# Kernel tuning notes

Measured on AMD Instinct MI355X. Metric: run time of the kernel, lower is better.

The kernel has to match this reference:

```python
import jax, jax.numpy as jnp
import numpy as np

B, C, H, W = 16, 256, 112, 112
WS, HEADS, HIDDEN = 7, 4, 512  # window_size, num_heads, int(dim*mlp_ratio)
EPS = 1e-5


def _layernorm(x, g, b):
    m = jnp.mean(x, axis=-1, keepdims=True)
    v = jnp.mean(jnp.square(x - m), axis=-1, keepdims=True)
    return (x - m) * jax.lax.rsqrt(v + EPS) * g + b


def setup_inputs() -> dict:
    key = jax.random.key(0)
    ks = jax.random.split(key, 6)
    s = 0.02
    return {
        "x": jax.random.normal(ks[0], (B, C, H, W), jnp.float32),
        "ln1_g": jnp.ones((C,), jnp.float32),
        "ln1_b": jnp.zeros((C,), jnp.float32),
        "qkv_w": jax.random.normal(ks[1], (C, 3 * C), jnp.float32) * s,
        "qkv_b": jnp.zeros((3 * C,), jnp.float32),
        "proj_w": jax.random.normal(ks[2], (C, C), jnp.float32) * s,
        "proj_b": jnp.zeros((C,), jnp.float32),
        "ln2_g": jnp.ones((C,), jnp.float32),
        "ln2_b": jnp.zeros((C,), jnp.float32),
        "mlp_w1": jax.random.normal(ks[3], (C, HIDDEN), jnp.float32) * s,
        "mlp_b1": jnp.zeros((HIDDEN,), jnp.float32),
        "mlp_w2": jax.random.normal(ks[4], (HIDDEN, C), jnp.float32) * s,
        "mlp_b2": jnp.zeros((C,), jnp.float32),
    }


def reference(x, ln1_g, ln1_b, qkv_w, qkv_b, proj_w, proj_b,
              ln2_g, ln2_b, mlp_w1, mlp_b1, mlp_w2, mlp_b2):
    nh, nw = H // WS, W // WS  # H,W divisible by WS -> no padding branch
    T = WS * WS               # 49 tokens per window
    d = C // HEADS
    # window partition: (B,C,H,W) -> (B*nh*nw, T, C)
    win = x.reshape(B, C, nh, WS, nw, WS).transpose(0, 2, 4, 3, 5, 1)
    win = win.reshape(B * nh * nw, T, C)
    # LN1 + MHA (pytorch nn.MultiheadAttention semantics)
    n1 = _layernorm(win, ln1_g, ln1_b)
    qkv = n1 @ qkv_w + qkv_b
    q, k, v = jnp.split(qkv, 3, axis=-1)
    N = win.shape[0]
    q = q.reshape(N, T, HEADS, d)
    k = k.reshape(N, T, HEADS, d)
    v = v.reshape(N, T, HEADS, d)
    scores = jnp.einsum('nthd,nshd->nhts', q, k) / jnp.sqrt(jnp.float32(d))
    attn = jax.nn.softmax(scores, axis=-1)
    o = jnp.einsum('nhts,nshd->nthd', attn, v).reshape(N, T, C)
    o = o @ proj_w + proj_b
    win = win + o
    # LN2 + MLP (exact erf GELU, matching nn.GELU default)
    n2 = _layernorm(win, ln2_g, ln2_b)
    hmid = jax.nn.gelu(n2 @ mlp_w1 + mlp_b1, approximate=False)
    win = win + (hmid @ mlp_w2 + mlp_b2)
    # window reverse: (B*nh*nw, T, C) -> (B,C,H,W)
    y = win.reshape(B, nh, nw, WS, WS, C).transpose(0, 5, 1, 3, 2, 4)
    return y.reshape(B, C, H, W)
```

## Files before the change

kernel.cpp:

```cpp
#include <hip/hip_runtime.h>
#include <hip/hip_bf16.h>

typedef __bf16 bf16x8 __attribute__((ext_vector_type(8)));
typedef float  f32x4  __attribute__((ext_vector_type(4)));
typedef unsigned short u16x8 __attribute__((ext_vector_type(8)));

#define CH    256
#define IMG   112
#define WSZ   7
#define TOK   49
#define NWIN  4096
#define HID   512
#define NTHR  512

#define SX_ST 260

#define OFF_AF   51200
#define OFF_V    51200
#define OFF_Q    83968
#define OFF_P    83968
#define PSZ      7168
#define OFF_HM   83968
#define OFF_K    116736
#define OFF_OF   116736
#define OFF_MR   149504
#define OFF_PRM  150016
#define OFF_PART 154112
#define SMEM_SZ  157248

#define WS_PROJ_BLK 384
#define WS_W1_BLK   512
#define WS_W2_BLK   768

__device__ __forceinline__ unsigned short f2bf(float f) {
    __bf16 h = (__bf16)f;
    return __builtin_bit_cast(unsigned short, h);
}

__device__ __forceinline__ f32x4 mfma16(bf16x8 a, bf16x8 b, f32x4 c) {
    return __builtin_amdgcn_mfma_f32_16x16x32_bf16(a, b, c, 0, 0, 0);
}

__device__ __forceinline__ int frOff(int base, int t, int c) {
    return base + (((t >> 4) * 8 + (c >> 5)) << 10)
                + (((((c >> 3) & 3) << 4) | (t & 15)) << 4)
                + ((c & 7) << 1);
}
__device__ __forceinline__ int frOffT(int base, int c, int t) {
    return base + ((((c >> 4) << 1) + (t >> 5)) << 10)
                + (((((t >> 3) & 3) << 4) | (c & 15)) << 4)
                + ((t & 7) << 1);
}

extern "C" __global__ __launch_bounds__(64)
void prepack(const float* __restrict__ qkv_w, const float* __restrict__ proj_w,
             const float* __restrict__ w1, const float* __restrict__ w2,
             char* __restrict__ ws)
{
    const int blk = blockIdx.x, l = threadIdx.x;
    const float* W; int nt, kt, ncols;
    if (blk < WS_PROJ_BLK)      { W = qkv_w;  int i = blk;               nt = i >> 3; kt = i & 7;  ncols = 768; }
    else if (blk < WS_W1_BLK)   { W = proj_w; int i = blk - WS_PROJ_BLK; nt = i >> 3; kt = i & 7;  ncols = 256; }
    else if (blk < WS_W2_BLK)   { W = w1;     int i = blk - WS_W1_BLK;   nt = i >> 3; kt = i & 7;  ncols = 512; }
    else                        { W = w2;     int i = blk - WS_W2_BLK;   nt = i >> 4; kt = i & 15; ncols = 256; }
    const int n  = nt * 16 + (l & 15);
    const int k0 = kt * 32 + (l >> 4) * 8;
    u16x8 o;
    #pragma unroll
    for (int j = 0; j < 8; ++j) o[j] = f2bf(W[(size_t)(k0 + j) * ncols + n]);
    *(u16x8*)(ws + (size_t)blk * 1024 + l * 16) = o;
}

extern "C" __global__ __launch_bounds__(NTHR, 1)
void swin_block(const float* __restrict__ x,
                const float* __restrict__ ln1_g, const float* __restrict__ ln1_b,
                const float* __restrict__ qkv_b,
                const float* __restrict__ proj_b,
                const float* __restrict__ ln2_g, const float* __restrict__ ln2_b,
                const float* __restrict__ b1, const float* __restrict__ b2,
                const char* __restrict__ ws,
                float* __restrict__ y)
{
    __shared__ __align__(16) char smem[SMEM_SZ];
    float*  sX = (float*)(smem + 0);
    float*  sM = (float*)(smem + OFF_MR);
    float*  sR = sM + 64;
    float*  sG1 = (float*)(smem + OFF_PRM);
    float*  sB1 = sG1 + 256;
    float*  sG2 = sB1 + 256;
    float*  sB2 = sG2 + 256;
    float2* sPart = (float2*)(smem + OFF_PART);

    const int tid  = threadIdx.x;
    const int wid  = tid >> 6;
    const int lane = tid & 63;
    const int sub  = lane >> 4;
    const int l15  = lane & 15;
    const int li7  = lane / 7;
    const int lj7  = lane - li7 * 7;

    const int n  = blockIdx.x;
    const int b  = n >> 8;
    const int wh = (n >> 4) & 15;
    const int ww = n & 15;
    const int row0 = wh * WSZ, col0 = ww * WSZ;
    const size_t xbase = (size_t)b * CH * IMG * IMG;

    const f32x4 z4 = {0.f, 0.f, 0.f, 0.f};

    bf16x8 pbF0[8];

    {
        float ps1 = 0.f, ps2 = 0.f;
        if (lane < TOK) {
            const float* xs = x + xbase + (size_t)(row0 + li7) * IMG + (col0 + lj7);
            float* dst = sX + lane * SX_ST;
            #pragma unroll 8
            for (int c = wid; c < CH; c += 8) {
                float v = xs[(size_t)c * (IMG * IMG)];
                dst[c] = v;
                ps1 += v; ps2 += v * v;
            }
        }
        int t2 = tid & 255;
        if (tid < 256) { sG1[t2] = ln1_g[t2]; sB1[t2] = ln1_b[t2]; }
        else           { sG2[t2] = ln2_g[t2]; sB2[t2] = ln2_b[t2]; }
        if (lane < TOK) sPart[lane * 8 + wid] = make_float2(ps1, ps2);
    }
    __syncthreads();

    if (tid < TOK) {
        float s1 = 0.f, s2 = 0.f;
        #pragma unroll
        for (int w = 0; w < 8; ++w) {
            float2 q = sPart[tid * 8 + w];
            s1 += q.x; s2 += q.y;
        }
        float m = s1 * (1.f / 256.f);
        float var = s2 * (1.f / 256.f) - m * m;
        sM[tid] = m; sR[tid] = rsqrtf(var + 1e-5f);
    }
    __syncthreads();

    bf16x8 bA[8], bB[8];
    #pragma unroll
    for (int kt = 0; kt < 8; ++kt)
        bA[kt] = *(const bf16x8*)(ws + (size_t)(((wid * 6) * 8 + kt) << 10) + lane * 16);

    for (int e = tid; e < 2048; e += NTHR) {
        int t = e & 63, cb = e >> 6;
        char* dst = smem + OFF_AF + (((t >> 4) * 8 + (cb >> 2)) << 10)
                  + (((((cb & 3) << 4) | (t & 15))) << 4);
        if (t < TOK) {
            const float* xr = sX + t * SX_ST + cb * 8;
            float4 xa = *(const float4*)xr;
            float4 xb = *(const float4*)(xr + 4);
            float m = sM[t], rs = sR[t];
            int c = cb * 8;
            u16x8 o;
            o[0] = f2bf((xa.x - m) * rs * sG1[c + 0] + sB1[c + 0]);
            o[1] = f2bf((xa.y - m) * rs * sG1[c + 1] + sB1[c + 1]);
            o[2] = f2bf((xa.z - m) * rs * sG1[c + 2] + sB1[c + 2]);
            o[3] = f2bf((xa.w - m) * rs * sG1[c + 3] + sB1[c + 3]);
            o[4] = f2bf((xb.x - m) * rs * sG1[c + 4] + sB1[c + 4]);
            o[5] = f2bf((xb.y - m) * rs * sG1[c + 5] + sB1[c + 5]);
            o[6] = f2bf((xb.z - m) * rs * sG1[c + 6] + sB1[c + 6]);
            o[7] = f2bf((xb.w - m) * rs * sG1[c + 7] + sB1[c + 7]);
            *(u16x8*)dst = o;
        } else {
            u16x8 z = {0, 0, 0, 0, 0, 0, 0, 0};
            *(u16x8*)dst = z;
        }
    }
    __syncthreads();

    {
        bf16x8 aF[4][8];
        #pragma unroll
        for (int mt = 0; mt < 4; ++mt)
            #pragma unroll
            for (int kt = 0; kt < 8; ++kt)
                aF[mt][kt] = *(const bf16x8*)(smem + OFF_AF + ((mt * 8 + kt) << 10) + lane * 16);
        __syncthreads();

        auto qkv_epi = [&](int ntg, const f32x4 (&acc)[4]) {
            const float bias = qkv_b[ntg * 16 + l15];
            const int m3 = ntg >> 4;
            const int c = (ntg & 15) * 16 + l15;
            if (m3 == 2) {
                #pragma unroll
                for (int mt = 0; mt < 4; ++mt)
                    #pragma unroll
                    for (int r = 0; r < 4; ++r) {
                        int t = mt * 16 + sub * 4 + r;
                        *(unsigned short*)(smem + frOffT(OFF_V, c, t)) = f2bf(acc[mt][r] + bias);
                    }
            } else if (m3 == 1) {
                #pragma unroll
                for (int mt = 0; mt < 4; ++mt)
                    #pragma unroll
                    for (int r = 0; r < 4; ++r) {
                        int t = mt * 16 + sub * 4 + r;
                        *(unsigned short*)(smem + frOff(OFF_K, t, c)) = f2bf(acc[mt][r] + bias);
                    }
            } else {
                #pragma unroll
                for (int mt = 0; mt < 4; ++mt)
                    #pragma unroll
                    for (int r = 0; r < 4; ++r) {
                        int t = mt * 16 + sub * 4 + r;
                        *(unsigned short*)(smem + frOff(OFF_Q, t, c)) = f2bf((acc[mt][r] + bias) * 0.125f);
                    }
            }
        };

        for (int i = 0; i < 6; i += 2) {
            const int n0 = wid * 6 + i;
            #pragma unroll
            for (int kt = 0; kt < 8; ++kt)
                bB[kt] = *(const bf16x8*)(ws + (size_t)(((n0 + 1) * 8 + kt) << 10) + lane * 16);
            {
                f32x4 acc[4] = {z4, z4, z4, z4};
                #pragma unroll
                for (int kt = 0; kt < 8; ++kt)
                    #pragma unroll
                    for (int mt = 0; mt < 4; ++mt)
                        acc[mt] = mfma16(aF[mt][kt], bA[kt], acc[mt]);
                qkv_epi(n0, acc);
            }
            if (i + 2 < 6) {
                #pragma unroll
                for (int kt = 0; kt < 8; ++kt)
                    bA[kt] = *(const bf16x8*)(ws + (size_t)(((n0 + 2) * 8 + kt) << 10) + lane * 16);
            }
            {
                f32x4 acc[4] = {z4, z4, z4, z4};
                #pragma unroll
                for (int kt = 0; kt < 8; ++kt)
                    #pragma unroll
                    for (int mt = 0; mt < 4; ++mt)
                        acc[mt] = mfma16(aF[mt][kt], bB[kt], acc[mt]);
                qkv_epi(n0 + 1, acc);
            }
        }
    }
    __syncthreads();

    {
        const int h  = wid >> 1;
        const int ah = wid & 1;
        f32x4 sc[2][4];
        #pragma unroll
        for (int m = 0; m < 2; ++m)
            #pragma unroll
            for (int nt = 0; nt < 4; ++nt) sc[m][nt] = z4;

        {
            bf16x8 qf[2][2], kf[4][2];
            #pragma unroll
            for (int m = 0; m < 2; ++m)
                #pragma unroll
                for (int k2 = 0; k2 < 2; ++k2)
                    qf[m][k2] = *(const bf16x8*)(smem + OFF_Q + (((ah * 2 + m) * 8 + h * 2 + k2) << 10) + lane * 16);
            #pragma unroll
            for (int nt = 0; nt < 4; ++nt)
                #pragma unroll
                for (int k2 = 0; k2 < 2; ++k2)
                    kf[nt][k2] = *(const bf16x8*)(smem + OFF_K + ((nt * 8 + h * 2 + k2) << 10) + lane * 16);
            #pragma unroll
            for (int k2 = 0; k2 < 2; ++k2)
                #pragma unroll
                for (int m = 0; m < 2; ++m)
                    #pragma unroll
                    for (int nt = 0; nt < 4; ++nt)
                        sc[m][nt] = mfma16(qf[m][k2], kf[nt][k2], sc[m][nt]);
        }
        __syncthreads();

        #pragma unroll
        for (int kt = 0; kt < 8; ++kt)
            pbF0[kt] = *(const bf16x8*)(ws + (size_t)(((WS_PROJ_BLK + (wid * 2) * 8 + kt)) << 10) + lane * 16);

        const int pbase = OFF_P + h * PSZ;
        #pragma unroll
        for (int m = 0; m < 2; ++m) {
            #pragma unroll
            for (int r = 0; r < 4; ++r) {
                const int t = (ah * 2 + m) * 16 + sub * 4 + r;
                float v0 = sc[m][0][r];
                float v1 = sc[m][1][r];
                float v2 = sc[m][2][r];
                float v3 = (l15 == 0) ? sc[m][3][r] : -1e30f;
                float mx = fmaxf(fmaxf(v0, v1), fmaxf(v2, v3));
                mx = fmaxf(mx, __shfl_xor(mx, 1));
                mx = fmaxf(mx, __shfl_xor(mx, 2));
                mx = fmaxf(mx, __shfl_xor(mx, 4));
                mx = fmaxf(mx, __shfl_xor(mx, 8));
                float e0 = __expf(v0 - mx), e1 = __expf(v1 - mx);
                float e2 = __expf(v2 - mx), e3 = __expf(v3 - mx);
                float s = e0 + e1 + e2 + e3;
                s += __shfl_xor(s, 1);
                s += __shfl_xor(s, 2);
                s += __shfl_xor(s, 4);
                s += __shfl_xor(s, 8);
                float inv = 1.f / s;
                if (t < TOK) {
                    unsigned short* pr = (unsigned short*)(smem + pbase + t * 144);
                    pr[l15]      = f2bf(e0 * inv);
                    pr[16 + l15] = f2bf(e1 * inv);
                    pr[32 + l15] = f2bf(e2 * inv);
                    pr[48 + l15] = f2bf(e3 * inv);
                }
            }
        }

        bf16x8 pf[2][2], vf[4][2];
        #pragma unroll
        for (int m = 0; m < 2; ++m)
            #pragma unroll
            for (int k2 = 0; k2 < 2; ++k2) {
                int row = (ah * 2 + m) * 16 + l15; row = row > 48 ? 48 : row;
                pf[m][k2] = *(const bf16x8*)(smem + pbase + row * 144 + ((k2 * 32 + sub * 8) << 1));
            }
        #pragma unroll
        for (int nt = 0; nt < 4; ++nt)
            #pragma unroll
            for (int k2 = 0; k2 < 2; ++k2)
                vf[nt][k2] = *(const bf16x8*)(smem + OFF_V + ((((h * 4 + nt) << 1) + k2) << 10) + lane * 16);

        f32x4 oc[2][4];
        #pragma unroll
        for (int m = 0; m < 2; ++m)
            #pragma unroll
            for (int nt = 0; nt < 4; ++nt) oc[m][nt] = z4;
        #pragma unroll
        for (int k2 = 0; k2 < 2; ++k2)
            #pragma unroll
            for (int m = 0; m < 2; ++m)
                #pragma unroll
                for (int nt = 0; nt < 4; ++nt)
                    oc[m][nt] = mfma16(pf[m][k2], vf[nt][k2], oc[m][nt]);
        #pragma unroll
        for (int m = 0; m < 2; ++m)
            #pragma unroll
            for (int nt = 0; nt < 4; ++nt)
                #pragma unroll
                for (int r = 0; r < 4; ++r) {
                    int t = (ah * 2 + m) * 16 + sub * 4 + r;
                    int c = h * 64 + nt * 16 + l15;
                    *(unsigned short*)(smem + frOff(OFF_OF, t, c)) = f2bf(oc[m][nt][r]);
                }
    }
    __syncthreads();

    float* sW = sX;
    {
        bf16x8 pbF1[8];
        #pragma unroll
        for (int kt = 0; kt < 8; ++kt)
            pbF1[kt] = *(const bf16x8*)(ws + (size_t)(((WS_PROJ_BLK + (wid * 2 + 1) * 8 + kt)) << 10) + lane * 16);

        bf16x8 aF[4][8];
        #pragma unroll
        for (int mt = 0; mt < 4; ++mt)
            #pragma unroll
            for (int kt = 0; kt < 8; ++kt)
                aF[mt][kt] = *(const bf16x8*)(smem + OFF_OF + ((mt * 8 + kt) << 10) + lane * 16);

        auto proj_epi = [&](int ntg, const f32x4 (&acc)[4]) {
            const int c = ntg * 16 + l15;
            const float bias = proj_b[c];
            #pragma unroll
            for (int mt = 0; mt < 4; ++mt)
                #pragma unroll
                for (int r = 0; r < 4; ++r) {
                    int t = mt * 16 + sub * 4 + r;
                    if (t < TOK) sW[t * SX_ST + c] += acc[mt][r] + bias;
                }
        };

        {
            f32x4 acc[4] = {z4, z4, z4, z4};
            #pragma unroll
            for (int kt = 0; kt < 8; ++kt)
                #pragma unroll
                for (int mt = 0; mt < 4; ++mt)
                    acc[mt] = mfma16(aF[mt][kt], pbF0[kt], acc[mt]);
            proj_epi(wid * 2, acc);
        }
        {
            f32x4 acc[4] = {z4, z4, z4, z4};
            #pragma unroll
            for (int kt = 0; kt < 8; ++kt)
                #pragma unroll
                for (int mt = 0; mt < 4; ++mt)
                    acc[mt] = mfma16(aF[mt][kt], pbF1[kt], acc[mt]);
            proj_epi(wid * 2 + 1, acc);
        }
    }
    __syncthreads();

    for (int t = wid; t < TOK; t += 8) {
        const float4 v = *(const float4*)&sW[t * SX_ST + lane * 4];
        float s1 = v.x + v.y + v.z + v.w;
        float s2 = v.x * v.x + v.y * v.y + v.z * v.z + v.w * v.w;
        #pragma unroll
        for (int off = 32; off > 0; off >>= 1) {
            s1 += __shfl_xor(s1, off);
            s2 += __shfl_xor(s2, off);
        }
        if (lane == 0) {
            float m = s1 * (1.f / 256.f);
            float var = s2 * (1.f / 256.f) - m * m;
            sM[t] = m; sR[t] = rsqrtf(var + 1e-5f);
        }
    }
    __syncthreads();

    for (int e = tid; e < 2048; e += NTHR) {
        int t = e & 63, cb = e >> 6;
        char* dst = smem + OFF_AF + (((t >> 4) * 8 + (cb >> 2)) << 10)
                  + (((((cb & 3) << 4) | (t & 15))) << 4);
        if (t < TOK) {
            const float* xr = sW + t * SX_ST + cb * 8;
            float4 xa = *(const float4*)xr;
            float4 xb = *(const float4*)(xr + 4);
            float m = sM[t], rs = sR[t];
            int c = cb * 8;
            u16x8 o;
            o[0] = f2bf((xa.x - m) * rs * sG2[c + 0] + sB2[c + 0]);
            o[1] = f2bf((xa.y - m) * rs * sG2[c + 1] + sB2[c + 1]);
            o[2] = f2bf((xa.z - m) * rs * sG2[c + 2] + sB2[c + 2]);
            o[3] = f2bf((xa.w - m) * rs * sG2[c + 3] + sB2[c + 3]);
            o[4] = f2bf((xb.x - m) * rs * sG2[c + 4] + sB2[c + 4]);
            o[5] = f2bf((xb.y - m) * rs * sG2[c + 5] + sB2[c + 5]);
            o[6] = f2bf((xb.z - m) * rs * sG2[c + 6] + sB2[c + 6]);
            o[7] = f2bf((xb.w - m) * rs * sG2[c + 7] + sB2[c + 7]);
            *(u16x8*)dst = o;
        } else {
            u16x8 z = {0, 0, 0, 0, 0, 0, 0, 0};
            *(u16x8*)dst = z;
        }
    }
    __syncthreads();

    {
        f32x4 acc2[2][4];
        #pragma unroll
        for (int i = 0; i < 2; ++i)
            #pragma unroll
            for (int mt = 0; mt < 4; ++mt) acc2[i][mt] = z4;

        for (int half = 0; half < 2; ++half) {
            {
                bf16x8 bF0[8], bF1[8];
                #pragma unroll
                for (int kt = 0; kt < 8; ++kt) {
                    bF0[kt] = *(const bf16x8*)(ws + (size_t)(((WS_W1_BLK + (half * 16 + wid * 2) * 8 + kt)) << 10) + lane * 16);
                    bF1[kt] = *(const bf16x8*)(ws + (size_t)(((WS_W1_BLK + (half * 16 + wid * 2 + 1) * 8 + kt)) << 10) + lane * 16);
                }

                #pragma unroll
                for (int mh = 0; mh < 2; ++mh) {
                    bf16x8 nf[2][8];
                    #pragma unroll
                    for (int mm = 0; mm < 2; ++mm)
                        #pragma unroll
                        for (int kt = 0; kt < 8; ++kt)
                            nf[mm][kt] = *(const bf16x8*)(smem + OFF_AF + (((mh * 2 + mm) * 8 + kt) << 10) + lane * 16);

                    f32x4 a0[2] = {z4, z4}, a1[2] = {z4, z4};
                    #pragma unroll
                    for (int kt = 0; kt < 8; ++kt)
                        #pragma unroll
                        for (int mm = 0; mm < 2; ++mm) {
                            a0[mm] = mfma16(nf[mm][kt], bF0[kt], a0[mm]);
                            a1[mm] = mfma16(nf[mm][kt], bF1[kt], a1[mm]);
                        }

                    #pragma unroll
                    for (int tile = 0; tile < 2; ++tile) {
                        const int ntg = wid * 2 + tile;
                        const int chm = ntg * 16 + l15;
                        const float bias = b1[half * 256 + chm];
                        #pragma unroll
                        for (int mm = 0; mm < 2; ++mm)
                            #pragma unroll
                            for (int r = 0; r < 4; ++r) {
                                int t = (mh * 2 + mm) * 16 + sub * 4 + r;
                                if (t < TOK) {
                                    float v = (tile ? a1[mm][r] : a0[mm][r]) + bias;
                                    float u = v * (1.5957691216f + 0.07135481627f * v * v);
                                    float g = v / (1.f + __expf(-u));
                                    *(unsigned short*)(smem + frOff(OFF_HM, t, chm)) = f2bf(g);
                                }
                            }
                    }
                }
            }
            __syncthreads();

            {
                bf16x8 bF0[8], bF1[8];
                #pragma unroll
                for (int kt = 0; kt < 8; ++kt) {
                    bF0[kt] = *(const bf16x8*)(ws + (size_t)(((WS_W2_BLK + (wid * 2 + 0) * 16 + half * 8 + kt)) << 10) + lane * 16);
                    bF1[kt] = *(const bf16x8*)(ws + (size_t)(((WS_W2_BLK + (wid * 2 + 1) * 16 + half * 8 + kt)) << 10) + lane * 16);
                }
                #pragma unroll
                for (int mh = 0; mh < 2; ++mh) {
                    bf16x8 hf[2][8];
                    #pragma unroll
                    for (int mm = 0; mm < 2; ++mm)
                        #pragma unroll
                        for (int kt = 0; kt < 8; ++kt)
                            hf[mm][kt] = *(const bf16x8*)(smem + OFF_HM + (((mh * 2 + mm) * 8 + kt) << 10) + lane * 16);
                    #pragma unroll
                    for (int kt = 0; kt < 8; ++kt)
                        #pragma unroll
                        for (int mm = 0; mm < 2; ++mm) {
                            acc2[0][mh * 2 + mm] = mfma16(hf[mm][kt], bF0[kt], acc2[0][mh * 2 + mm]);
                            acc2[1][mh * 2 + mm] = mfma16(hf[mm][kt], bF1[kt], acc2[1][mh * 2 + mm]);
                        }
                }
            }
            __syncthreads();
        }

        #pragma unroll
        for (int i = 0; i < 2; ++i) {
            const int c = (wid * 2 + i) * 16 + l15;
            const float bias = b2[c];
            #pragma unroll
            for (int mt = 0; mt < 4; ++mt)
                #pragma unroll
                for (int r = 0; r < 4; ++r) {
                    int t = mt * 16 + sub * 4 + r;
                    if (t < TOK) sW[t * SX_ST + c] += acc2[i][mt][r] + bias;
                }
        }
    }
    __syncthreads();

    if (lane < TOK) {
        float* ys = y + xbase + (size_t)(row0 + li7) * IMG + (col0 + lj7);
        const float* src = sW + lane * SX_ST;
        #pragma unroll 8
        for (int c = wid; c < CH; c += 8)
            ys[(size_t)c * (IMG * IMG)] = src[c];
    }
}

extern "C" void kernel_launch(void* const* d_in, const int* in_sizes, int n_in,
                              void* d_out, int out_size, void* d_ws, size_t ws_size,
                              hipStream_t stream) {
    const float* x      = (const float*)d_in[0];
    const float* ln1_g  = (const float*)d_in[1];
    const float* ln1_b  = (const float*)d_in[2];
    const float* qkv_w  = (const float*)d_in[3];
    const float* qkv_b  = (const float*)d_in[4];
    const float* proj_w = (const float*)d_in[5];
    const float* proj_b = (const float*)d_in[6];
    const float* ln2_g  = (const float*)d_in[7];
    const float* ln2_b  = (const float*)d_in[8];
    const float* w1     = (const float*)d_in[9];
    const float* b1     = (const float*)d_in[10];
    const float* w2     = (const float*)d_in[11];
    const float* b2     = (const float*)d_in[12];

    hipLaunchKernelGGL(prepack, dim3(1024), dim3(64), 0, stream,
                       qkv_w, proj_w, w1, w2, (char*)d_ws);
    hipLaunchKernelGGL(swin_block, dim3(NWIN), dim3(NTHR), 0, stream,
                       x, ln1_g, ln1_b, qkv_b, proj_b, ln2_g, ln2_b, b1, b2,
                       (const char*)d_ws, (float*)d_out);
}
```

Baseline: 732.8 us.

## Fuse LN2 statistics into projection epilogue and remap block-to-window order

The LN2 mean and variance partial sums are now computed inside the projection epilogue with 16-lane shuffles and written per wave into sPart. A small 49-thread reduction then replaces the separate pass that reread the whole residual tile from shared memory. Block indices are also permuted so that consecutive blocks take windows spread across the grid, which may change cache and channel locality. The cost is more shuffles in the epilogue, plus a read-modify-write of sPart that relies on each wave owning its own slot.

```diff
diff --git a/kernel.cpp b/kernel.cpp
--- a/kernel.cpp
+++ b/kernel.cpp
@@ -99,7 +99,8 @@
     const int li7  = lane / 7;
     const int lj7  = lane - li7 * 7;
 
-    const int n  = blockIdx.x;
+    const int bid = blockIdx.x;
+    const int n  = (bid & 7) * (NWIN / 8) + (bid >> 3);
     const int b  = n >> 8;
     const int wh = (n >> 4) & 15;
     const int ww = n & 15;
@@ -367,7 +368,7 @@
             for (int kt = 0; kt < 8; ++kt)
                 aF[mt][kt] = *(const bf16x8*)(smem + OFF_OF + ((mt * 8 + kt) << 10) + lane * 16);
 
-        auto proj_epi = [&](int ntg, const f32x4 (&acc)[4]) {
+        auto proj_epi = [&](int ntg, const f32x4 (&acc)[4], bool first) {
             const int c = ntg * 16 + l15;
             const float bias = proj_b[c];
             #pragma unroll
@@ -375,7 +376,23 @@
                 #pragma unroll
                 for (int r = 0; r < 4; ++r) {
                     int t = mt * 16 + sub * 4 + r;
-                    if (t < TOK) sW[t * SX_ST + c] += acc[mt][r] + bias;
+                    if (t < TOK) {
+                        float w = sW[t * SX_ST + c] + acc[mt][r] + bias;
+                        sW[t * SX_ST + c] = w;
+                        float a = w, bb = w * w;
+                        a += __shfl_xor(a, 1); bb += __shfl_xor(bb, 1);
+                        a += __shfl_xor(a, 2); bb += __shfl_xor(bb, 2);
+                        a += __shfl_xor(a, 4); bb += __shfl_xor(bb, 4);
+                        a += __shfl_xor(a, 8); bb += __shfl_xor(bb, 8);
+                        if (l15 == 0) {
+                            if (first) {
+                                sPart[t * 8 + wid] = make_float2(a, bb);
+                            } else {
+                                float2 q = sPart[t * 8 + wid];
+                                sPart[t * 8 + wid] = make_float2(q.x + a, q.y + bb);
+                            }
+                        }
+                    }
                 }
         };
 
@@ -386,7 +403,7 @@
                 #pragma unroll
                 for (int mt = 0; mt < 4; ++mt)
                     acc[mt] = mfma16(aF[mt][kt], pbF0[kt], acc[mt]);
-            proj_epi(wid * 2, acc);
+            proj_epi(wid * 2, acc, true);
         }
         {
             f32x4 acc[4] = {z4, z4, z4, z4};
@@ -395,25 +412,21 @@
                 #pragma unroll
                 for (int mt = 0; mt < 4; ++mt)
                     acc[mt] = mfma16(aF[mt][kt], pbF1[kt], acc[mt]);
-            proj_epi(wid * 2 + 1, acc);
-        }
-    }
-    __syncthreads();
-
-    for (int t = wid; t < TOK; t += 8) {
-        const float4 v = *(const float4*)&sW[t * SX_ST + lane * 4];
-        float s1 = v.x + v.y + v.z + v.w;
-        float s2 = v.x * v.x + v.y * v.y + v.z * v.z + v.w * v.w;
-        #pragma unroll
-        for (int off = 32; off > 0; off >>= 1) {
-            s1 += __shfl_xor(s1, off);
-            s2 += __shfl_xor(s2, off);
-        }
-        if (lane == 0) {
-            float m = s1 * (1.f / 256.f);
-            float var = s2 * (1.f / 256.f) - m * m;
-            sM[t] = m; sR[t] = rsqrtf(var + 1e-5f);
-        }
+            proj_epi(wid * 2 + 1, acc, false);
+        }
+    }
+    __syncthreads();
+
+    if (tid < TOK) {
+        float s1 = 0.f, s2 = 0.f;
+        #pragma unroll
+        for (int w = 0; w < 8; ++w) {
+            float2 q = sPart[tid * 8 + w];
+            s1 += q.x; s2 += q.y;
+        }
+        float m = s1 * (1.f / 256.f);
+        float var = s2 * (1.f / 256.f) - m * m;
+        sM[tid] = m; sR[tid] = rsqrtf(var + 1e-5f);
     }
     __syncthreads();
 
```

Measured after the change: 683.9 us. -6.7%, faster.
